# Performance work log

Hardware: AMD Instinct MI355X
Metric: run time of the kernel (lower is better)

The kernel has to match this reference:

```python
import jax, jax.numpy as jnp
import numpy as np
import math

D, H, FF = 1024, 16, 4096
B, L = 4, 1024

def setup_inputs() -> dict:
    key = jax.random.key(0)
    ks = jax.random.split(key, 20)
    g = lambda k, shp: jax.random.normal(k, shp, dtype=jnp.float32) * 0.02
    inp = {
        'x': jax.random.normal(ks[0], (B, L, D), dtype=jnp.float32),
        'encoder_output': jax.random.normal(ks[1], (B, L, D), dtype=jnp.float32),
        'src_mask': jnp.ones((1, 1, L, L), dtype=jnp.int32),
        'tgt_mask': jnp.tril(jnp.ones((L, L), dtype=jnp.int32))[None, None],
        'wq': g(ks[2], (D, D)), 'bq': jnp.zeros((D,), jnp.float32),
        'wk': g(ks[3], (D, D)), 'bk': jnp.zeros((D,), jnp.float32),
        'wv': g(ks[4], (D, D)), 'bv': jnp.zeros((D,), jnp.float32),
        'wo': g(ks[5], (D, D)), 'bo': jnp.zeros((D,), jnp.float32),
        'w1': g(ks[6], (FF, D)), 'b1': jnp.zeros((FF,), jnp.float32),
        'w2': g(ks[7], (D, FF)), 'b2': jnp.zeros((D,), jnp.float32),
        'g1': jnp.ones((D,), jnp.float32), 'be1': jnp.zeros((D,), jnp.float32),
        'g2': jnp.ones((D,), jnp.float32), 'be2': jnp.zeros((D,), jnp.float32),
    }
    return inp

def _layernorm(x, g, b, eps=1e-5):
    mu = jnp.mean(x, axis=-1, keepdims=True)
    var = jnp.var(x, axis=-1, keepdims=True)
    return (x - mu) * jax.lax.rsqrt(var + eps) * g + b

def _mha(q, k, v, mask, wq, bq, wk, bk, wv, bv, wo, bo):
    Bq, Lq, C = q.shape
    dh = C // H
    qh = (q @ wq.T + bq).reshape(Bq, Lq, H, dh)      # b q h d
    kh = (k @ wk.T + bk).reshape(Bq, -1, H, dh)       # b k h d
    vh = (v @ wv.T + bv).reshape(Bq, -1, H, dh)
    # NOTE: source scales by sqrt(C) (full model dim), not sqrt(head_dim)
    scores = jnp.einsum('bqhd,bkhd->bhqk', qh, kh) / math.sqrt(C)
    if mask is not None:
        scores = jnp.where(mask == 0, jnp.float32(-1e9), scores)
    attn = jax.nn.softmax(scores, axis=-1)
    out = jnp.einsum('bhqk,bkhd->bqhd', attn, vh).reshape(Bq, Lq, C)
    return out @ wo.T + bo

def reference(x, encoder_output, src_mask, tgt_mask,
              wq, bq, wk, bk, wv, bv, wo, bo,
              w1, b1, w2, b2, g1, be1, g2, be2):
    # self-attention (dropout identity in eval mode)
    y1 = _mha(x, x, x, tgt_mask, wq, bq, wk, bk, wv, bv, wo, bo)
    y1 = _layernorm(y1 + x, g1, be1)
    # cross-attention: source reuses attn1 weights and layer_norm1 (faithful)
    y2 = _mha(y1, encoder_output, encoder_output, src_mask, wq, bq, wk, bk, wv, bv, wo, bo)
    y2 = _layernorm(y1 + y2, g1, be1)
    # FFN + layer_norm2
    y = jax.nn.relu(y2 @ w1.T + b1) @ w2.T + b2
    return _layernorm(y2 + y, g2, be2)
```

## Files before the change

kernel.cpp:

```cpp
#include <hip/hip_runtime.h>
#include <hip/hip_bf16.h>

typedef __attribute__((ext_vector_type(8))) short short8;
typedef __attribute__((ext_vector_type(4))) float f32x4;
typedef __attribute__((ext_vector_type(4))) unsigned short ushort4v;

#define MFMA_BF16(a, b, c) __builtin_amdgcn_mfma_f32_16x16x32_bf16((a), (b), (c), 0, 0, 0)
#define AS1 __attribute__((address_space(1)))
#define AS3 __attribute__((address_space(3)))

__device__ __forceinline__ unsigned short f2b(float f) {
  unsigned u = __float_as_uint(f);
  u += 0x7fffu + ((u >> 16) & 1u);
  return (unsigned short)(u >> 16);
}

__device__ __forceinline__ size_t kpack_idx(int row, int col) {
  int b = row >> 10, l = row & 1023, h = col >> 6, d = col & 63;
  return ((size_t)(b * 16 + h) << 16) + l * 64 + (d ^ ((l & 7) << 3));
}

__global__ __launch_bounds__(256) void cast8(
    const float* s0, const float* s1, const float* s2, const float* s3,
    const float* s4, const float* s5, const float* s6, const float* s7,
    unsigned short* d0, unsigned short* d1, unsigned short* d2, unsigned short* d3,
    unsigned short* d4, unsigned short* d5, unsigned short* d6, unsigned short* d7,
    int n0, int n1, int n2, int n3, int n4, int n5, int n6, int n7) {
  const float* s; unsigned short* d; int n;
  switch (blockIdx.y) {
    case 0: s = s0; d = d0; n = n0; break;
    case 1: s = s1; d = d1; n = n1; break;
    case 2: s = s2; d = d2; n = n2; break;
    case 3: s = s3; d = d3; n = n3; break;
    case 4: s = s4; d = d4; n = n4; break;
    case 5: s = s5; d = d5; n = n5; break;
    case 6: s = s6; d = d6; n = n6; break;
    default: s = s7; d = d7; n = n7; break;
  }
  int stride = gridDim.x * blockDim.x;
  for (int i = blockIdx.x * blockDim.x + threadIdx.x; i < n; i += stride) {
    float4 v = reinterpret_cast<const float4*>(s)[i];
    ushort4v o;
    o.x = f2b(v.x); o.y = f2b(v.y); o.z = f2b(v.z); o.w = f2b(v.w);
    reinterpret_cast<ushort4v*>(d)[i] = o;
  }
}

template <int RELU, int RES, int OUTF, int OUTB, int TM>
__global__ __launch_bounds__(256) void gemm_bt(
    const unsigned short* __restrict__ A, const unsigned short* __restrict__ W,
    const float* __restrict__ bias, const float* __restrict__ resid,
    float* __restrict__ outF, unsigned short* __restrict__ outB,
    int M, int N, int K) {
  constexpr int MI = TM / 32;
  __shared__ unsigned short lA[TM * 64];
  __shared__ unsigned short lB[128 * 64];
  int nbn = N >> 7;
  int nwg = gridDim.x;
  int id = blockIdx.x;
  { int q = nwg >> 3; id = (id & 7) * q + (id >> 3); }
  int m0 = (id / nbn) * TM, n0 = (id % nbn) << 7;
  int lane = threadIdx.x & 63, wave = threadIdx.x >> 6;
  int wr = (wave >> 1) * (TM / 2), wc = (wave & 1) * 64;
  int rq = lane & 15, kq = (lane >> 4) * 8;
  int xr8 = (rq & 7) << 3;
  f32x4 acc[MI][4] = {};

  int t8 = threadIdx.x * 8;
  for (int kt = 0; kt < K; kt += 64) {
#pragma unroll
    for (int i = 0; i < MI; ++i) {
      int e = t8 + i * 2048;
      int row = e >> 6;
      int gcol = (((e >> 3) & 7) ^ (row & 7)) << 3;
      __builtin_amdgcn_global_load_lds(
          (const AS1 void*)(A + (size_t)(m0 + row) * K + kt + gcol),
          (AS3 void*)(lA + e), 16, 0, 0);
    }
#pragma unroll
    for (int i = 0; i < 4; ++i) {
      int e = t8 + i * 2048;
      int row = e >> 6;
      int gcol = (((e >> 3) & 7) ^ (row & 7)) << 3;
      __builtin_amdgcn_global_load_lds(
          (const AS1 void*)(W + (size_t)(n0 + row) * K + kt + gcol),
          (AS3 void*)(lB + e), 16, 0, 0);
    }
    __syncthreads();
#pragma unroll
    for (int s = 0; s < 2; ++s) {
      short8 af[MI], bf[4];
#pragma unroll
      for (int i = 0; i < MI; ++i)
        af[i] = *reinterpret_cast<const short8*>(lA + (wr + i * 16 + rq) * 64 + ((s * 32 + kq) ^ xr8));
#pragma unroll
      for (int j = 0; j < 4; ++j)
        bf[j] = *reinterpret_cast<const short8*>(lB + (wc + j * 16 + rq) * 64 + ((s * 32 + kq) ^ xr8));
#pragma unroll
      for (int i = 0; i < MI; ++i)
#pragma unroll
        for (int j = 0; j < 4; ++j)
          acc[i][j] = MFMA_BF16(af[i], bf[j], acc[i][j]);
    }
    __syncthreads();
  }

  int r0 = (lane >> 4) * 4;
#pragma unroll
  for (int i = 0; i < MI; ++i) {
#pragma unroll
    for (int j = 0; j < 4; ++j) {
      int row = m0 + wr + i * 16 + r0;
      int col = n0 + wc + j * 16 + rq;
      float bv = bias[col];
#pragma unroll
      for (int r = 0; r < 4; ++r) {
        float v = acc[i][j][r] + bv;
        if (RES) v += resid[(size_t)(row + r) * N + col];
        if (RELU) v = fmaxf(v, 0.0f);
        if (OUTF) outF[(size_t)(row + r) * N + col] = v;
        if (OUTB) outB[(size_t)(row + r) * N + col] = f2b(v);
      }
    }
  }
}

__global__ __launch_bounds__(256, 2) void gemm_qkv_f(
    const unsigned short* __restrict__ xb, const unsigned short* __restrict__ encb,
    const unsigned short* __restrict__ wq, const unsigned short* __restrict__ wk,
    const unsigned short* __restrict__ wv,
    const float* __restrict__ bq, const float* __restrict__ bk, const float* __restrict__ bv,
    unsigned short* __restrict__ qb, unsigned short* __restrict__ kp1,
    unsigned short* __restrict__ vp1, unsigned short* __restrict__ kp2,
    unsigned short* __restrict__ vp2) {
  __shared__ unsigned short lA[2][4096];
  __shared__ unsigned short lB[2][3][4096];
  int id = blockIdx.x;
  id = (id & 7) * 64 + (id >> 3);
  int sel = id >> 8;
  int idx = id & 255;
  int m0 = (idx >> 3) << 7, col0 = (idx & 7) << 7;
  int nW = sel ? 2 : 3;
  const unsigned short* A = sel ? encb : xb;
  const unsigned short* W0 = sel ? wk : wq;
  const unsigned short* W1 = sel ? wv : wk;
  const unsigned short* W2 = wv;
  int lane = threadIdx.x & 63, wave = threadIdx.x >> 6;
  int wr = (wave >> 1) * 64, wc = (wave & 1) * 64;
  int rq = lane & 15, kq = (lane >> 4) * 8;
  f32x4 acc[3][4][4] = {};

  int e0 = threadIdx.x * 8;
#define STG(KT, BUF)                                                            \
  {                                                                             \
    _Pragma("unroll") for (int i = 0; i < 2; ++i) {                             \
      int e = e0 + i * 2048;                                                    \
      int row = e >> 5, col = e & 31;                                           \
      __builtin_amdgcn_global_load_lds(                                         \
          (const AS1 void*)(A + (size_t)(m0 + row) * 1024 + (KT) + col),        \
          (AS3 void*)(&lA[BUF][e]), 16, 0, 0);                                  \
      __builtin_amdgcn_global_load_lds(                                         \
          (const AS1 void*)(W0 + (size_t)(col0 + row) * 1024 + (KT) + col),     \
          (AS3 void*)(&lB[BUF][0][e]), 16, 0, 0);                               \
      __builtin_amdgcn_global_load_lds(                                         \
          (const AS1 void*)(W1 + (size_t)(col0 + row) * 1024 + (KT) + col),     \
          (AS3 void*)(&lB[BUF][1][e]), 16, 0, 0);                               \
      if (!sel)                                                                 \
        __builtin_amdgcn_global_load_lds(                                       \
            (const AS1 void*)(W2 + (size_t)(col0 + row) * 1024 + (KT) + col),   \
            (AS3 void*)(&lB[BUF][2][e]), 16, 0, 0);                             \
    }                                                                           \
  }

  STG(0, 0);
  __syncthreads();
  for (int t = 0; t < 32; ++t) {
    int cur = t & 1;
    if (t + 1 < 32) STG((t + 1) << 5, cur ^ 1);
    short8 af[4];
#pragma unroll
    for (int i = 0; i < 4; ++i)
      af[i] = *reinterpret_cast<const short8*>(&lA[cur][(wr + i * 16 + rq) * 32 + kq]);
#pragma unroll
    for (int w = 0; w < 3; ++w) {
      if (w < nW) {
        short8 bf[4];
#pragma unroll
        for (int j = 0; j < 4; ++j)
          bf[j] = *reinterpret_cast<const short8*>(&lB[cur][w][(wc + j * 16 + rq) * 32 + kq]);
#pragma unroll
        for (int i = 0; i < 4; ++i)
#pragma unroll
          for (int j = 0; j < 4; ++j)
            acc[w][i][j] = MFMA_BF16(af[i], bf[j], acc[w][i][j]);
      }
    }
    __syncthreads();
  }
#undef STG

  int r0 = (lane >> 4) * 4;
#pragma unroll
  for (int w = 0; w < 3; ++w) {
    if (w >= nW) continue;
    const float* bias = sel ? (w == 0 ? bk : bv) : (w == 0 ? bq : (w == 1 ? bk : bv));
    unsigned short* outp = sel ? (w == 0 ? kp2 : vp2) : (w == 0 ? qb : (w == 1 ? kp1 : vp1));
    int pack = sel ? (w + 1) : w;
#pragma unroll
    for (int i = 0; i < 4; ++i) {
#pragma unroll
      for (int j = 0; j < 4; ++j) {
        int row0 = m0 + wr + i * 16 + r0;
        int col = col0 + wc + j * 16 + rq;
        float bv2 = bias[col];
        if (pack == 2) {
          int b = row0 >> 10, k0 = row0 & 1023, h = col >> 6, d = col & 63;
          size_t idx2 = ((size_t)((b * 16 + h) * 16 + (k0 >> 6)) << 12) + d * 64 + ((k0 & 63) ^ ((d & 7) << 3));
          ushort4v o;
          o.x = f2b(acc[w][i][j][0] + bv2);
          o.y = f2b(acc[w][i][j][1] + bv2);
          o.z = f2b(acc[w][i][j][2] + bv2);
          o.w = f2b(acc[w][i][j][3] + bv2);
          *reinterpret_cast<ushort4v*>(&outp[idx2]) = o;
        } else {
#pragma unroll
          for (int r = 0; r < 4; ++r) {
            int row = row0 + r;
            float v = acc[w][i][j][r] + bv2;
            if (pack == 0) outp[(size_t)row * 1024 + col] = f2b(v);
            else outp[kpack_idx(row, col)] = f2b(v);
          }
        }
      }
    }
  }
}

__device__ __forceinline__ void attn_step(
    const unsigned short* __restrict__ kcur, const unsigned short* __restrict__ vcur,
    unsigned short* __restrict__ plw, const short8* qf,
    f32x4* accd, float& m2, float& lsum,
    int rq, int hi, int kq, int xr, int wave, bool domask) {
  const float SC = 0.04508422f;
  f32x4 st[4];
  __builtin_amdgcn_s_setprio(1);
#pragma unroll
  for (int sub = 0; sub < 4; ++sub) {
    f32x4 z = {0.f, 0.f, 0.f, 0.f};
#pragma unroll
    for (int c = 0; c < 2; ++c) {
      short8 kf = *reinterpret_cast<const short8*>(
          &kcur[(sub * 16 + rq) * 64 + ((c * 32 + hi * 8) ^ xr)]);
      z = MFMA_BF16(kf, qf[c], z);
    }
    st[sub] = z * SC;
  }
  __builtin_amdgcn_s_setprio(0);
  if (domask) {
#pragma unroll
    for (int sub = 0; sub < 4; ++sub)
#pragma unroll
      for (int r = 0; r < 4; ++r)
        if (sub * 16 + hi * 4 + r > wave * 16 + rq) st[sub][r] = -1e9f;
  }
  f32x4 t0 = {fmaxf(st[0][0], st[1][0]), fmaxf(st[0][1], st[1][1]),
              fmaxf(st[0][2], st[1][2]), fmaxf(st[0][3], st[1][3])};
  f32x4 t1 = {fmaxf(st[2][0], st[3][0]), fmaxf(st[2][1], st[3][1]),
              fmaxf(st[2][2], st[3][2]), fmaxf(st[2][3], st[3][3])};
  float mx = fmaxf(fmaxf(fmaxf(t0[0], t1[0]), fmaxf(t0[1], t1[1])),
                   fmaxf(fmaxf(t0[2], t1[2]), fmaxf(t0[3], t1[3])));
  mx = fmaxf(mx, __shfl_xor(mx, 16, 64));
  mx = fmaxf(mx, __shfl_xor(mx, 32, 64));
  float mn = fmaxf(m2, mx);
  float al = exp2f(m2 - mn);
  m2 = mn;
  f32x4 e[4];
#pragma unroll
  for (int sub = 0; sub < 4; ++sub)
#pragma unroll
    for (int r = 0; r < 4; ++r) e[sub][r] = exp2f(st[sub][r] - mn);
  f32x4 s01 = e[0] + e[1], s23 = e[2] + e[3];
  f32x4 s = s01 + s23;
  float ps = (s[0] + s[1]) + (s[2] + s[3]);
  ps += __shfl_xor(ps, 16, 64);
  ps += __shfl_xor(ps, 32, 64);
  lsum = lsum * al + ps;
#pragma unroll
  for (int sub = 0; sub < 4; ++sub) {
    unsigned w0 = (unsigned)f2b(e[sub][0]) | ((unsigned)f2b(e[sub][1]) << 16);
    unsigned w1 = (unsigned)f2b(e[sub][2]) | ((unsigned)f2b(e[sub][3]) << 16);
    uint2 w = make_uint2(w0, w1);
    *reinterpret_cast<uint2*>(&plw[rq * 64 + ((sub * 16 + hi * 4) ^ xr)]) = w;
  }
  float alb[4];
#pragma unroll
  for (int r = 0; r < 4; ++r) alb[r] = __shfl(al, hi * 4 + r, 64);
#pragma unroll
  for (int d = 0; d < 4; ++d)
#pragma unroll
    for (int r = 0; r < 4; ++r) accd[d][r] *= alb[r];
  short8 pf[2];
#pragma unroll
  for (int c = 0; c < 2; ++c)
    pf[c] = *reinterpret_cast<const short8*>(&plw[rq * 64 + ((c * 32 + hi * 8) ^ xr)]);
  __builtin_amdgcn_s_setprio(1);
#pragma unroll
  for (int d = 0; d < 4; ++d) {
#pragma unroll
    for (int c = 0; c < 2; ++c) {
      short8 vf = *reinterpret_cast<const short8*>(
          &vcur[(d * 16 + rq) * 64 + ((c * 32 + hi * 8) ^ xr)]);
      accd[d] = MFMA_BF16(pf[c], vf, accd[d]);
    }
  }
  __builtin_amdgcn_s_setprio(0);
}

__global__ __launch_bounds__(256) void attn_kernel(
    const unsigned short* __restrict__ Q, const unsigned short* __restrict__ Kp,
    const unsigned short* __restrict__ Vp, unsigned short* __restrict__ O, int causal) {
  __shared__ unsigned short kls[2][4096];
  __shared__ unsigned short vls[2][4096];
  __shared__ unsigned short pls[4][1024];
  int id = blockIdx.x;
  int xcd = id & 7, j = id >> 3;
  int bh = xcd * 8 + (j & 7);
  int b = bh >> 4, h = bh & 15;
  int lane = threadIdx.x & 63, wave = threadIdx.x >> 6;
  int rq = lane & 15, hi = lane >> 4, kq = hi * 8;
  int xr = (rq & 7) << 3;
  int sb = wave * 1024 + lane * 8;
  const unsigned short* Kbh = Kp + ((size_t)bh << 16);
  const unsigned short* Vbh = Vp + ((size_t)bh << 16);
  unsigned short* plw = pls[wave];

  int p = j >> 3;
  int qtA = p;
  int qtB = causal ? (15 - p) : (p + 8);
  int lastA = causal ? qtA : 15;
  int nkt = causal ? (qtB + 1) : 16;

  int qrowA = qtA * 64 + wave * 16, qrowB = qtB * 64 + wave * 16;
  short8 qfA[2], qfB[2];
#pragma unroll
  for (int c = 0; c < 2; ++c) {
    qfA[c] = *reinterpret_cast<const short8*>(
        Q + (size_t)(b * 1024 + qrowA + rq) * 1024 + h * 64 + c * 32 + kq);
    qfB[c] = *reinterpret_cast<const short8*>(
        Q + (size_t)(b * 1024 + qrowB + rq) * 1024 + h * 64 + c * 32 + kq);
  }

  float mA = -1e30f, lsA = 0.f, mB = -1e30f, lsB = 0.f;
  f32x4 accA[4] = {}, accB[4] = {};

#pragma unroll
  for (int i = 0; i < 2; ++i) {
    __builtin_amdgcn_global_load_lds((const AS1 void*)(Kbh + sb + i * 512),
                                     (AS3 void*)(&kls[0][sb + i * 512]), 16, 0, 0);
    __builtin_amdgcn_global_load_lds((const AS1 void*)(Vbh + sb + i * 512),
                                     (AS3 void*)(&vls[0][sb + i * 512]), 16, 0, 0);
  }
  __syncthreads();

  int cur = 0;
  for (int kt = 0; kt < nkt; ++kt) {
    if (kt + 1 < nkt) {
      const unsigned short* kg = Kbh + (kt + 1) * 4096 + sb;
      const unsigned short* vg = Vbh + (kt + 1) * 4096 + sb;
#pragma unroll
      for (int i = 0; i < 2; ++i) {
        __builtin_amdgcn_global_load_lds((const AS1 void*)(kg + i * 512),
                                         (AS3 void*)(&kls[cur ^ 1][sb + i * 512]), 16, 0, 0);
        __builtin_amdgcn_global_load_lds((const AS1 void*)(vg + i * 512),
                                         (AS3 void*)(&vls[cur ^ 1][sb + i * 512]), 16, 0, 0);
      }
    }
    attn_step(kls[cur], vls[cur], plw, qfB, accB, mB, lsB, rq, hi, kq, xr, wave,
              causal && kt == qtB);
    if (kt <= lastA)
      attn_step(kls[cur], vls[cur], plw, qfA, accA, mA, lsA, rq, hi, kq, xr, wave,
                causal && kt == qtA);
    __syncthreads();
    cur ^= 1;
  }

  float lbA[4], lbB[4];
#pragma unroll
  for (int r = 0; r < 4; ++r) {
    lbA[r] = 1.0f / __shfl(lsA, hi * 4 + r, 64);
    lbB[r] = 1.0f / __shfl(lsB, hi * 4 + r, 64);
  }
#pragma unroll
  for (int d = 0; d < 4; ++d)
#pragma unroll
    for (int r = 0; r < 4; ++r) {
      O[(size_t)(b * 1024 + qrowA + hi * 4 + r) * 1024 + h * 64 + d * 16 + rq] =
          f2b(accA[d][r] * lbA[r]);
      O[(size_t)(b * 1024 + qrowB + hi * 4 + r) * 1024 + h * 64 + d * 16 + rq] =
          f2b(accB[d][r] * lbB[r]);
    }
}

template <int OUTF, int OUTB>
__global__ __launch_bounds__(256) void ln_kernel(const float* __restrict__ X,
                                                 const float* __restrict__ g,
                                                 const float* __restrict__ be,
                                                 float* __restrict__ outF,
                                                 unsigned short* __restrict__ outB) {
  __shared__ float red[2][4];
  int row = blockIdx.x;
  int t = threadIdx.x;
  const float* xr = X + (size_t)row * 1024;
  float4 v = reinterpret_cast<const float4*>(xr)[t];
  float s = v.x + v.y + v.z + v.w;
  float ss = v.x * v.x + v.y * v.y + v.z * v.z + v.w * v.w;
#pragma unroll
  for (int off = 1; off < 64; off <<= 1) {
    s += __shfl_xor(s, off, 64);
    ss += __shfl_xor(ss, off, 64);
  }
  int wave = t >> 6;
  if ((t & 63) == 0) { red[0][wave] = s; red[1][wave] = ss; }
  __syncthreads();
  s = red[0][0] + red[0][1] + red[0][2] + red[0][3];
  ss = red[1][0] + red[1][1] + red[1][2] + red[1][3];
  float mu = s * (1.f / 1024.f);
  float var = ss * (1.f / 1024.f) - mu * mu;
  float rs = rsqrtf(var + 1e-5f);
  float4 gv = reinterpret_cast<const float4*>(g)[t];
  float4 bv = reinterpret_cast<const float4*>(be)[t];
  float o0 = (v.x - mu) * rs * gv.x + bv.x;
  float o1 = (v.y - mu) * rs * gv.y + bv.y;
  float o2 = (v.z - mu) * rs * gv.z + bv.z;
  float o3 = (v.w - mu) * rs * gv.w + bv.w;
  if (OUTF) {
    float4 o = make_float4(o0, o1, o2, o3);
    reinterpret_cast<float4*>(outF + (size_t)row * 1024)[t] = o;
  }
  if (OUTB) {
    ushort4v o;
    o.x = f2b(o0); o.y = f2b(o1); o.z = f2b(o2); o.w = f2b(o3);
    reinterpret_cast<ushort4v*>(outB + (size_t)row * 1024)[t] = o;
  }
}

extern "C" void kernel_launch(void* const* d_in, const int* in_sizes, int n_in,
                              void* d_out, int out_size, void* d_ws, size_t ws_size,
                              hipStream_t stream) {
  const float* x   = (const float*)d_in[0];
  const float* enc = (const float*)d_in[1];
  const float* wq = (const float*)d_in[4];  const float* bq = (const float*)d_in[5];
  const float* wk = (const float*)d_in[6];  const float* bk = (const float*)d_in[7];
  const float* wv = (const float*)d_in[8];  const float* bv = (const float*)d_in[9];
  const float* wo = (const float*)d_in[10]; const float* bo = (const float*)d_in[11];
  const float* w1 = (const float*)d_in[12]; const float* b1 = (const float*)d_in[13];
  const float* w2 = (const float*)d_in[14]; const float* b2 = (const float*)d_in[15];
  const float* g1 = (const float*)d_in[16]; const float* be1 = (const float*)d_in[17];
  const float* g2 = (const float*)d_in[18]; const float* be2 = (const float*)d_in[19];
  float* out = (float*)d_out;

  const int M = 4096;
  char* ws = (char*)d_ws;
  size_t off = 0;
  auto alloc = [&](size_t bytes) -> char* {
    char* p = ws + off;
    off += (bytes + 255) & ~(size_t)255;
    return p;
  };
  unsigned short* xb   = (unsigned short*)alloc((size_t)M * 1024 * 2);
  unsigned short* encb = (unsigned short*)alloc((size_t)M * 1024 * 2);
  unsigned short* wqb  = (unsigned short*)alloc((size_t)1024 * 1024 * 2);
  unsigned short* wkb  = (unsigned short*)alloc((size_t)1024 * 1024 * 2);
  unsigned short* wvb  = (unsigned short*)alloc((size_t)1024 * 1024 * 2);
  unsigned short* wob  = (unsigned short*)alloc((size_t)1024 * 1024 * 2);
  unsigned short* w1b  = (unsigned short*)alloc((size_t)4096 * 1024 * 2);
  unsigned short* w2b  = (unsigned short*)alloc((size_t)4096 * 1024 * 2);
  unsigned short* qb   = (unsigned short*)alloc((size_t)M * 1024 * 2);
  unsigned short* kp1  = (unsigned short*)alloc((size_t)M * 1024 * 2);
  unsigned short* vp1  = (unsigned short*)alloc((size_t)M * 1024 * 2);
  unsigned short* kp2  = (unsigned short*)alloc((size_t)M * 1024 * 2);
  unsigned short* vp2  = (unsigned short*)alloc((size_t)M * 1024 * 2);
  unsigned short* ab   = (unsigned short*)alloc((size_t)M * 1024 * 2);
  float* s1 = (float*)alloc((size_t)M * 1024 * 4);
  float* y1 = (float*)alloc((size_t)M * 1024 * 4);
  unsigned short* hb = kp1;
  unsigned short* y1b = xb;
  unsigned short* y2b = qb;
  float* y2 = y1;

  dim3 b256(256);
  cast8<<<dim3(256, 8), b256, 0, stream>>>(
      x, enc, wq, wk, wv, wo, w1, w2,
      xb, encb, wqb, wkb, wvb, wob, w1b, w2b,
      M * 1024 / 4, M * 1024 / 4, 262144, 262144, 262144, 262144,
      4096 * 1024 / 4, 4096 * 1024 / 4);

  gemm_qkv_f<<<512, b256, 0, stream>>>(xb, encb, wqb, wkb, wvb, bq, bk, bv,
                                       qb, kp1, vp1, kp2, vp2);

  attn_kernel<<<512, b256, 0, stream>>>(qb, kp1, vp1, ab, 1);
  gemm_bt<0, 1, 1, 0, 64><<<512, b256, 0, stream>>>(ab, wob, bo, x, s1, nullptr, M, 1024, 1024);
  ln_kernel<1, 1><<<4096, b256, 0, stream>>>(s1, g1, be1, y1, y1b);

  gemm_bt<0, 0, 0, 1, 64><<<512, b256, 0, stream>>>(y1b, wqb, bq, nullptr, nullptr, qb, M, 1024, 1024);
  attn_kernel<<<512, b256, 0, stream>>>(qb, kp2, vp2, ab, 0);
  gemm_bt<0, 1, 1, 0, 64><<<512, b256, 0, stream>>>(ab, wob, bo, y1, s1, nullptr, M, 1024, 1024);
  ln_kernel<1, 1><<<4096, b256, 0, stream>>>(s1, g1, be1, y2, y2b);

  gemm_bt<1, 0, 0, 1, 128><<<1024, b256, 0, stream>>>(y2b, w1b, b1, nullptr, nullptr, hb, M, 4096, 1024);
  gemm_bt<0, 1, 1, 0, 64><<<512, b256, 0, stream>>>(hb, w2b, b2, y2, s1, nullptr, M, 1024, 4096);
  ln_kernel<1, 0><<<4096, b256, 0, stream>>>(s1, g2, be2, out, nullptr);

  (void)in_sizes; (void)n_in; (void)out_size; (void)ws_size;
}
```

Before: 341.5 us.

## Split-K the FFN down-projection and swizzle LDS layout in QKV GEMM

The FFN second GEMM (K=4096) is split into two K halves over 1024 workgroups. Each half writes its partial sums to a separate fp32 buffer, and a new layernorm kernel adds both partials to the residual before normalizing. This is meant to raise occupancy and parallelism for the long-K GEMM, at the cost of an extra M×N fp32 write and read. Separately, the fused QKV GEMM applies an XOR swizzle to its 32-wide LDS tiles to reduce bank conflicts on the fragment reads.

```diff
diff --git a/kernel.cpp b/kernel.cpp
--- a/kernel.cpp
+++ b/kernel.cpp
@@ -46,7 +46,7 @@
   }
 }
 
-template <int RELU, int RES, int OUTF, int OUTB, int TM>
+template <int RELU, int RES, int OUTF, int OUTB, int TM, int SPLITK>
 __global__ __launch_bounds__(256) void gemm_bt(
     const unsigned short* __restrict__ A, const unsigned short* __restrict__ W,
     const float* __restrict__ bias, const float* __restrict__ resid,
@@ -59,6 +59,8 @@
   int nwg = gridDim.x;
   int id = blockIdx.x;
   { int q = nwg >> 3; id = (id & 7) * q + (id >> 3); }
+  int half = 0;
+  if (SPLITK == 2) { half = id & 1; id >>= 1; }
   int m0 = (id / nbn) * TM, n0 = (id % nbn) << 7;
   int lane = threadIdx.x & 63, wave = threadIdx.x >> 6;
   int wr = (wave >> 1) * (TM / 2), wc = (wave & 1) * 64;
@@ -66,8 +68,10 @@
   int xr8 = (rq & 7) << 3;
   f32x4 acc[MI][4] = {};
 
+  int kBeg = (SPLITK == 2) ? half * (K >> 1) : 0;
+  int kEnd = (SPLITK == 2) ? kBeg + (K >> 1) : K;
   int t8 = threadIdx.x * 8;
-  for (int kt = 0; kt < K; kt += 64) {
+  for (int kt = kBeg; kt < kEnd; kt += 64) {
 #pragma unroll
     for (int i = 0; i < MI; ++i) {
       int e = t8 + i * 2048;
@@ -105,6 +109,7 @@
     __syncthreads();
   }
 
+  float* outFp = (SPLITK == 2) ? outF + (size_t)half * M * N : outF;
   int r0 = (lane >> 4) * 4;
 #pragma unroll
   for (int i = 0; i < MI; ++i) {
@@ -112,13 +117,13 @@
     for (int j = 0; j < 4; ++j) {
       int row = m0 + wr + i * 16 + r0;
       int col = n0 + wc + j * 16 + rq;
-      float bv = bias[col];
+      float bv = (SPLITK == 2 && half) ? 0.0f : bias[col];
 #pragma unroll
       for (int r = 0; r < 4; ++r) {
         float v = acc[i][j][r] + bv;
         if (RES) v += resid[(size_t)(row + r) * N + col];
         if (RELU) v = fmaxf(v, 0.0f);
-        if (OUTF) outF[(size_t)(row + r) * N + col] = v;
+        if (OUTF) outFp[(size_t)(row + r) * N + col] = v;
         if (OUTB) outB[(size_t)(row + r) * N + col] = f2b(v);
       }
     }
@@ -148,6 +153,7 @@
   int lane = threadIdx.x & 63, wave = threadIdx.x >> 6;
   int wr = (wave >> 1) * 64, wc = (wave & 1) * 64;
   int rq = lane & 15, kq = (lane >> 4) * 8;
+  int xk = ((rq >> 1) & 3) << 3;
   f32x4 acc[3][4][4] = {};
 
   int e0 = threadIdx.x * 8;
@@ -155,19 +161,20 @@
   {                                                                             \
     _Pragma("unroll") for (int i = 0; i < 2; ++i) {                             \
       int e = e0 + i * 2048;                                                    \
-      int row = e >> 5, col = e & 31;                                           \
+      int row = e >> 5;                                                         \
+      int gcol = ((((e >> 3) & 3) ^ ((row >> 1) & 3)) << 3);                    \
       __builtin_amdgcn_global_load_lds(                                         \
-          (const AS1 void*)(A + (size_t)(m0 + row) * 1024 + (KT) + col),        \
+          (const AS1 void*)(A + (size_t)(m0 + row) * 1024 + (KT) + gcol),       \
           (AS3 void*)(&lA[BUF][e]), 16, 0, 0);                                  \
       __builtin_amdgcn_global_load_lds(                                         \
-          (const AS1 void*)(W0 + (size_t)(col0 + row) * 1024 + (KT) + col),     \
+          (const AS1 void*)(W0 + (size_t)(col0 + row) * 1024 + (KT) + gcol),    \
           (AS3 void*)(&lB[BUF][0][e]), 16, 0, 0);                               \
       __builtin_amdgcn_global_load_lds(                                         \
-          (const AS1 void*)(W1 + (size_t)(col0 + row) * 1024 + (KT) + col),     \
+          (const AS1 void*)(W1 + (size_t)(col0 + row) * 1024 + (KT) + gcol),    \
           (AS3 void*)(&lB[BUF][1][e]), 16, 0, 0);                               \
       if (!sel)                                                                 \
         __builtin_amdgcn_global_load_lds(                                       \
-            (const AS1 void*)(W2 + (size_t)(col0 + row) * 1024 + (KT) + col),   \
+            (const AS1 void*)(W2 + (size_t)(col0 + row) * 1024 + (KT) + gcol),  \
             (AS3 void*)(&lB[BUF][2][e]), 16, 0, 0);                             \
     }                                                                           \
   }
@@ -180,14 +187,14 @@
     short8 af[4];
 #pragma unroll
     for (int i = 0; i < 4; ++i)
-      af[i] = *reinterpret_cast<const short8*>(&lA[cur][(wr + i * 16 + rq) * 32 + kq]);
+      af[i] = *reinterpret_cast<const short8*>(&lA[cur][(wr + i * 16 + rq) * 32 + (kq ^ xk)]);
 #pragma unroll
     for (int w = 0; w < 3; ++w) {
       if (w < nW) {
         short8 bf[4];
 #pragma unroll
         for (int j = 0; j < 4; ++j)
-          bf[j] = *reinterpret_cast<const short8*>(&lB[cur][w][(wc + j * 16 + rq) * 32 + kq]);
+          bf[j] = *reinterpret_cast<const short8*>(&lB[cur][w][(wc + j * 16 + rq) * 32 + (kq ^ xk)]);
 #pragma unroll
         for (int i = 0; i < 4; ++i)
 #pragma unroll
@@ -442,6 +449,42 @@
     o.x = f2b(o0); o.y = f2b(o1); o.z = f2b(o2); o.w = f2b(o3);
     reinterpret_cast<ushort4v*>(outB + (size_t)row * 1024)[t] = o;
   }
+}
+
+__global__ __launch_bounds__(256) void ln2_kernel(const float* __restrict__ Xa,
+                                                  const float* __restrict__ Xb,
+                                                  const float* __restrict__ R,
+                                                  const float* __restrict__ g,
+                                                  const float* __restrict__ be,
+                                                  float* __restrict__ outF) {
+  __shared__ float red[2][4];
+  int row = blockIdx.x;
+  int t = threadIdx.x;
+  float4 va = reinterpret_cast<const float4*>(Xa + (size_t)row * 1024)[t];
+  float4 vb = reinterpret_cast<const float4*>(Xb + (size_t)row * 1024)[t];
+  float4 vr = reinterpret_cast<const float4*>(R + (size_t)row * 1024)[t];
+  float4 v = make_float4(va.x + vb.x + vr.x, va.y + vb.y + vr.y,
+                         va.z + vb.z + vr.z, va.w + vb.w + vr.w);
+  float s = v.x + v.y + v.z + v.w;
+  float ss = v.x * v.x + v.y * v.y + v.z * v.z + v.w * v.w;
+#pragma unroll
+  for (int off = 1; off < 64; off <<= 1) {
+    s += __shfl_xor(s, off, 64);
+    ss += __shfl_xor(ss, off, 64);
+  }
+  int wave = t >> 6;
+  if ((t & 63) == 0) { red[0][wave] = s; red[1][wave] = ss; }
+  __syncthreads();
+  s = red[0][0] + red[0][1] + red[0][2] + red[0][3];
+  ss = red[1][0] + red[1][1] + red[1][2] + red[1][3];
+  float mu = s * (1.f / 1024.f);
+  float var = ss * (1.f / 1024.f) - mu * mu;
+  float rs = rsqrtf(var + 1e-5f);
+  float4 gv = reinterpret_cast<const float4*>(g)[t];
+  float4 bv = reinterpret_cast<const float4*>(be)[t];
+  float4 o = make_float4((v.x - mu) * rs * gv.x + bv.x, (v.y - mu) * rs * gv.y + bv.y,
+                         (v.z - mu) * rs * gv.z + bv.z, (v.w - mu) * rs * gv.w + bv.w);
+  reinterpret_cast<float4*>(outF + (size_t)row * 1024)[t] = o;
 }
 
 extern "C" void kernel_launch(void* const* d_in, const int* in_sizes, int n_in,
@@ -481,7 +524,7 @@
   unsigned short* kp2  = (unsigned short*)alloc((size_t)M * 1024 * 2);
   unsigned short* vp2  = (unsigned short*)alloc((size_t)M * 1024 * 2);
   unsigned short* ab   = (unsigned short*)alloc((size_t)M * 1024 * 2);
-  float* s1 = (float*)alloc((size_t)M * 1024 * 4);
+  float* s1 = (float*)alloc((size_t)2 * M * 1024 * 4);
   float* y1 = (float*)alloc((size_t)M * 1024 * 4);
   unsigned short* hb = kp1;
   unsigned short* y1b = xb;
@@ -499,17 +542,17 @@
                                        qb, kp1, vp1, kp2, vp2);
 
   attn_kernel<<<512, b256, 0, stream>>>(qb, kp1, vp1, ab, 1);
-  gemm_bt<0, 1, 1, 0, 64><<<512, b256, 0, stream>>>(ab, wob, bo, x, s1, nullptr, M, 1024, 1024);
+  gemm_bt<0, 1, 1, 0, 64, 1><<<512, b256, 0, stream>>>(ab, wob, bo, x, s1, nullptr, M, 1024, 1024);
   ln_kernel<1, 1><<<4096, b256, 0, stream>>>(s1, g1, be1, y1, y1b);
 
-  gemm_bt<0, 0, 0, 1, 64><<<512, b256, 0, stream>>>(y1b, wqb, bq, nullptr, nullptr, qb, M, 1024, 1024);
+  gemm_bt<0, 0, 0, 1, 64, 1><<<512, b256, 0, stream>>>(y1b, wqb, bq, nullptr, nullptr, qb, M, 1024, 1024);
   attn_kernel<<<512, b256, 0, stream>>>(qb, kp2, vp2, ab, 0);
-  gemm_bt<0, 1, 1, 0, 64><<<512, b256, 0, stream>>>(ab, wob, bo, y1, s1, nullptr, M, 1024, 1024);
+  gemm_bt<0, 1, 1, 0, 64, 1><<<512, b256, 0, stream>>>(ab, wob, bo, y1, s1, nullptr, M, 1024, 1024);
   ln_kernel<1, 1><<<4096, b256, 0, stream>>>(s1, g1, be1, y2, y2b);
 
-  gemm_bt<1, 0, 0, 1, 128><<<1024, b256, 0, stream>>>(y2b, w1b, b1, nullptr, nullptr, hb, M, 4096, 1024);
-  gemm_bt<0, 1, 1, 0, 64><<<512, b256, 0, stream>>>(hb, w2b, b2, y2, s1, nullptr, M, 1024, 4096);
-  ln_kernel<1, 0><<<4096, b256, 0, stream>>>(s1, g2, be2, out, nullptr);
+  gemm_bt<1, 0, 0, 1, 128, 1><<<1024, b256, 0, stream>>>(y2b, w1b, b1, nullptr, nullptr, hb, M, 4096, 1024);
+  gemm_bt<0, 0, 1, 0, 64, 2><<<1024, b256, 0, stream>>>(hb, w2b, b2, nullptr, s1, nullptr, M, 1024, 4096);
+  ln2_kernel<<<4096, b256, 0, stream>>>(s1, s1 + (size_t)M * 1024, y2, g2, be2, out);
 
   (void)in_sizes; (void)n_in; (void)out_size; (void)ws_size;
 }
```

Result: no change. 343.4 us (+0.6%).
